# Optimization experiments

Hardware: AMD Instinct MI355X
Metric: run time of the kernel (lower is better)

The kernel has to match this reference:

```python
import jax, jax.numpy as jnp
import numpy as np

B, C, L = 32, 8, 2048
K, S = 512, 64  # num_shapelets, shapelets_size


def setup_inputs() -> dict:
    key = jax.random.key(0)
    k1, k2 = jax.random.split(key)
    x = jax.random.normal(k1, (B, C, L), dtype=jnp.float32)
    shapelets = jax.random.normal(k2, (C, K, S), dtype=jnp.float32)
    return {"x": x, "shapelets": shapelets}


def reference(x, shapelets):
    # x: [B, C, L]; shapelets: [C, K, S]
    s = shapelets.shape[-1]
    n_dims = x.shape[1]
    W = x.shape[2] - s + 1  # number of sliding windows
    # unfold(2, S, 1): gather overlapping windows -> [B, C, W, S]
    idx = jnp.arange(W)[:, None] + jnp.arange(s)[None, :]
    xw = x[:, :, idx]
    # L2-normalize windows along window length (clamp min like torch)
    xw = xw / jnp.maximum(jnp.linalg.norm(xw, axis=-1, keepdims=True), 1e-8)
    # L2-normalize shapelets along length
    sn = shapelets / jnp.maximum(jnp.linalg.norm(shapelets, axis=-1, keepdims=True), 1e-8)
    # matmul [B,C,W,S] @ [C,S,K] then sum over C, fused into one einsum -> [B, W, K]
    sim = jnp.einsum('bcws,cks->bwk', xw, sn) / n_dims
    sim = jax.nn.relu(sim)
    # max over window positions -> [B, K]; keep the singleton channel dim like torch ([B,1,K])
    out = jnp.max(sim, axis=1)
    return out[:, None, :]
```

## Files before the change

### kernel.cpp

```cpp
#include <hip/hip_runtime.h>


#define B_ 32
#define C_ 8
#define L_ 2048
#define K_ 512
#define S_ 64
#define W_ 1985
#define XS_ 2176

typedef _Float16 f16x8  __attribute__((ext_vector_type(8)));
typedef _Float16 f16x8u __attribute__((ext_vector_type(8), aligned(4)));
typedef float    f32x16 __attribute__((ext_vector_type(16)));

__global__ __launch_bounds__(256)
void prep_k(const float* __restrict__ x, const float* __restrict__ sh,
            _Float16* __restrict__ Bp, float* __restrict__ invn,
            _Float16* __restrict__ xh0, _Float16* __restrict__ xh1,
            float* __restrict__ out) {
    __shared__ float xr[L_];
    const int tid = threadIdx.x;
    const int blk = blockIdx.x;

    if (blk < 128) {
        const int sb   = blk * 4 + (tid >> 6);
        const int c    = sb >> 6;
        const int kq   = (sb >> 4) & 3;
        const int nt   = sb & 15;
        const int lane = tid & 63;
        const int half = lane >> 5;
        const int q    = nt * 32 + (lane & 31);

        const float4* sp = (const float4*)(sh + (size_t)(c * K_ + q) * S_);
        float ss = 0.f;
        #pragma unroll
        for (int i = 0; i < 8; ++i) {
            float4 v = sp[half * 8 + i];
            ss += v.x * v.x + v.y * v.y + v.z * v.z + v.w * v.w;
        }
        ss += __shfl_xor(ss, 32);
        float inv = 1.f / fmaxf(sqrtf(ss), 1e-8f);

        float4 u0 = sp[kq * 4 + half * 2];
        float4 u1 = sp[kq * 4 + half * 2 + 1];
        f16x8 o;
        o[0] = (_Float16)(u0.x * inv); o[1] = (_Float16)(u0.y * inv);
        o[2] = (_Float16)(u0.z * inv); o[3] = (_Float16)(u0.w * inv);
        o[4] = (_Float16)(u1.x * inv); o[5] = (_Float16)(u1.y * inv);
        o[6] = (_Float16)(u1.z * inv); o[7] = (_Float16)(u1.w * inv);
        ((f16x8*)Bp)[((c * 4 + kq) * 16 + nt) * 64 + lane] = o;
    } else {
        const int r = blk - 128;
        const float* xp = x + (size_t)r * L_;
        for (int i = tid; i < L_ / 4; i += 256)
            ((float4*)xr)[i] = ((const float4*)xp)[i];
        __syncthreads();

        float* ivp = invn + (size_t)r * L_;
        const int w0 = tid * 8;
        float ss = 0.f;
        if (w0 < W_) {
            #pragma unroll
            for (int j = 0; j < S_; ++j) { float v = xr[w0 + j]; ss += v * v; }
        }
        #pragma unroll
        for (int u = 0; u < 8; ++u) {
            int w = w0 + u;
            float o = 0.f;
            if (u > 0 && w < W_)
                ss += xr[w + 63] * xr[w + 63] - xr[w - 1] * xr[w - 1];
            if (w < W_) o = 0.125f / fmaxf(sqrtf(ss), 1e-8f);
            if (w < L_) ivp[w] = o;
        }

        _Float16* p0 = xh0 + (size_t)r * XS_;
        _Float16* p1 = xh1 + (size_t)r * XS_;
        for (int i = tid; i < XS_ / 8; i += 256) {
            f16x8 o0, o1;
            #pragma unroll
            for (int j = 0; j < 8; ++j) {
                int e = i * 8 + j;
                o0[j] = (_Float16)((e     < L_) ? xr[e]     : 0.f);
                o1[j] = (_Float16)((e + 1 < L_) ? xr[e + 1] : 0.f);
            }
            ((f16x8*)p0)[i] = o0;
            ((f16x8*)p1)[i] = o1;
        }
        if (r < 64) out[r * 256 + tid] = 0.f;
    }
}

__device__ __forceinline__ void glds16(const void* g, void* l) {
    __builtin_amdgcn_global_load_lds(
        (const __attribute__((address_space(1))) unsigned int*)g,
        (__attribute__((address_space(3))) unsigned int*)l, 16, 0, 0);
}

__device__ __forceinline__ void loadA(
    int c, const _Float16* __restrict__ xbase, const float* __restrict__ ivbase,
    int m0, int m1, f16x8 (&ar)[8], float (&iv)[2])
{
    iv[0] = ivbase[(size_t)c * L_ + m0];
    iv[1] = ivbase[(size_t)c * L_ + m1];
    const _Float16* xp = xbase + (size_t)c * XS_;
    #pragma unroll
    for (int mt = 0; mt < 2; ++mt)
        #pragma unroll
        for (int ks = 0; ks < 4; ++ks)
            ar[mt * 4 + ks] = *(const f16x8u*)(xp + mt * 32 + ks * 16);
}

__device__ __forceinline__ void compC(
    const f16x8* __restrict__ bsl, int lane, int nw,
    const f16x8 (&ar)[8], const float (&iv)[2], f32x16 (&acc)[2][2])
{
    f16x8 bf[8];
    #pragma unroll
    for (int ks = 0; ks < 4; ++ks)
        #pragma unroll
        for (int nt = 0; nt < 2; ++nt)
            bf[ks * 2 + nt] = bsl[(ks * 4 + nw * 2 + nt) * 64 + lane];

    const _Float16 h0 = (_Float16)iv[0], h1 = (_Float16)iv[1];
    f16x8 is0, is1;
    #pragma unroll
    for (int j = 0; j < 8; ++j) { is0[j] = h0; is1[j] = h1; }

    #pragma unroll
    for (int ks = 0; ks < 4; ++ks) {
        f16x8 a0 = ar[0 * 4 + ks] * is0;
        f16x8 a1 = ar[1 * 4 + ks] * is1;
        #pragma unroll
        for (int nt = 0; nt < 2; ++nt) {
            acc[0][nt] = __builtin_amdgcn_mfma_f32_32x32x16_f16(
                a0, bf[ks * 2 + nt], acc[0][nt], 0, 0, 0);
            acc[1][nt] = __builtin_amdgcn_mfma_f32_32x32x16_f16(
                a1, bf[ks * 2 + nt], acc[1][nt], 0, 0, 0);
        }
    }
}

__global__ __launch_bounds__(256, 2)
void mcs_k(const _Float16* __restrict__ xh0, const _Float16* __restrict__ xh1,
           const _Float16* __restrict__ Bp, const float* __restrict__ invn,
           float* __restrict__ out) {
    const int wt  = blockIdx.x;
    const int ng  = blockIdx.y;
    const int b   = blockIdx.z;
    const int tid = threadIdx.x;
    const int lane = tid & 63;
    const int wv   = tid >> 6;
    const int mg   = wv >> 1;
    const int nw   = wv & 1;

    const int l31 = lane & 31;
    const int lh  = lane >> 5;
    const int Wb  = wt * 128 + mg * 64;
    const int m0  = Wb + l31;
    const int m1  = Wb + 32 + l31;

    __shared__ f16x8 Bs[2][16][64];
    __shared__ float red[2][2][32];

    const _Float16* xb = (l31 & 1) ? (xh1 - 1) : xh0;
    const _Float16* xbase = xb + (size_t)b * C_ * XS_ + Wb + l31 + lh * 8;
    const float*   ivbase = invn + (size_t)b * C_ * L_;
    const f16x8*   sg = (const f16x8*)Bp + ((wv * 16 + ng * 4) * 64) + lane;

    f32x16 acc[2][2];
    #pragma unroll
    for (int mt = 0; mt < 2; ++mt)
        #pragma unroll
        for (int nt = 0; nt < 2; ++nt)
            #pragma unroll
            for (int r = 0; r < 16; ++r) acc[mt][nt][r] = 0.f;

    f16x8 aA[8], aB[8];
    float ivA[2], ivB[2];

    #define STAGE(c, buf)                                              \
        { _Pragma("unroll")                                            \
          for (int u = 0; u < 4; ++u)                                  \
              glds16(sg + ((c) * 64 + u) * 64, &Bs[buf][wv * 4 + u][0]); }

    STAGE(0, 0);
    loadA(0, xbase, ivbase, m0, m1, aA, ivA);
    __syncthreads();

    #pragma unroll 1
    for (int cp = 0; cp < 4; ++cp) {
        const int c0 = cp * 2;
        STAGE(c0 + 1, 1);
        loadA(c0 + 1, xbase, ivbase, m0, m1, aB, ivB);
        compC(&Bs[0][0][0], lane, nw, aA, ivA, acc);
        __syncthreads();
        if (cp < 3) {
            STAGE(c0 + 2, 0);
            loadA(c0 + 2, xbase, ivbase, m0, m1, aA, ivA);
        }
        compC(&Bs[1][0][0], lane, nw, aB, ivB, acc);
        __syncthreads();
    }
    #undef STAGE

    float m[2];
    #pragma unroll
    for (int nt = 0; nt < 2; ++nt) {
        float v = 0.f;
        #pragma unroll
        for (int mt = 0; mt < 2; ++mt)
            #pragma unroll
            for (int r = 0; r < 16; ++r) v = fmaxf(v, acc[mt][nt][r]);
        v = fmaxf(v, __shfl_xor(v, 32));
        m[nt] = v;
    }

    if (mg == 0 && lane < 32) {
        red[nw][0][l31] = m[0];
        red[nw][1][l31] = m[1];
    }
    __syncthreads();
    if (mg == 1 && lane < 32) {
        #pragma unroll
        for (int nt = 0; nt < 2; ++nt) {
            float v = fmaxf(m[nt], red[nw][nt][l31]);
            atomicMax((unsigned int*)(out + (size_t)b * K_ + ng * 128 + nw * 64 + nt * 32 + l31),
                      __float_as_uint(v));
        }
    }
}

extern "C" void kernel_launch(void* const* d_in, const int* in_sizes, int n_in,
                              void* d_out, int out_size, void* d_ws, size_t ws_size,
                              hipStream_t stream) {
    const float* x  = (const float*)d_in[0];
    const float* sh = (const float*)d_in[1];
    float* out = (float*)d_out;

    _Float16* Bp   = (_Float16*)d_ws;
    float*    invn = (float*)((char*)d_ws + (512 << 10));
    _Float16* xh0  = (_Float16*)((char*)d_ws + (512 << 10) + (2 << 20));
    _Float16* xh1  = xh0 + (size_t)B_ * C_ * XS_;

    prep_k<<<dim3(384), dim3(256), 0, stream>>>(x, sh, Bp, invn, xh0, xh1, out);
    mcs_k<<<dim3(16, 4, B_), dim3(256), 0, stream>>>(xh0, xh1, Bp, invn, out);
}
```

Before: 99.50 us.

## Preload all-channel shapelet tile to LDS once and drop per-channel barriers

Each block now handles 256 windows by 64 shapelets. Every wave owns 64 windows and all 64 shapelets of the block, so no cross-wave reduction is needed. The shapelet B fragments for all 8 channels (64 KB) are loaded into LDS once at the start, which removes the per-channel double-buffered staging and the two __syncthreads per channel pair. MFMA sections are wrapped in s_setprio to favour matrix issue. The costs are more LDS per block, which may limit occupancy, and twice as many atomicMax writes, one per wave instead of a shared reduction.

```diff
diff --git a/kernel.cpp b/kernel.cpp
--- a/kernel.cpp
+++ b/kernel.cpp
@@ -111,7 +111,7 @@
 }
 
 __device__ __forceinline__ void compC(
-    const f16x8* __restrict__ bsl, int lane, int nw,
+    int c, const f16x8* __restrict__ bsl, int lane,
     const f16x8 (&ar)[8], const float (&iv)[2], f32x16 (&acc)[2][2])
 {
     f16x8 bf[8];
@@ -119,13 +119,14 @@
     for (int ks = 0; ks < 4; ++ks)
         #pragma unroll
         for (int nt = 0; nt < 2; ++nt)
-            bf[ks * 2 + nt] = bsl[(ks * 4 + nw * 2 + nt) * 64 + lane];
+            bf[ks * 2 + nt] = bsl[(c * 8 + ks * 2 + nt) * 64 + lane];
 
     const _Float16 h0 = (_Float16)iv[0], h1 = (_Float16)iv[1];
     f16x8 is0, is1;
     #pragma unroll
     for (int j = 0; j < 8; ++j) { is0[j] = h0; is1[j] = h1; }
 
+    __builtin_amdgcn_s_setprio(1);
     #pragma unroll
     for (int ks = 0; ks < 4; ++ks) {
         f16x8 a0 = ar[0 * 4 + ks] * is0;
@@ -138,6 +139,7 @@
                 a1, bf[ks * 2 + nt], acc[1][nt], 0, 0, 0);
         }
     }
+    __builtin_amdgcn_s_setprio(0);
 }
 
 __global__ __launch_bounds__(256, 2)
@@ -150,22 +152,30 @@
     const int tid = threadIdx.x;
     const int lane = tid & 63;
     const int wv   = tid >> 6;
-    const int mg   = wv >> 1;
-    const int nw   = wv & 1;
 
     const int l31 = lane & 31;
     const int lh  = lane >> 5;
-    const int Wb  = wt * 128 + mg * 64;
+    const int Wb  = wt * 256 + wv * 64;
     const int m0  = Wb + l31;
     const int m1  = Wb + 32 + l31;
 
-    __shared__ f16x8 Bs[2][16][64];
-    __shared__ float red[2][2][32];
+    __shared__ f16x8 Bs[64][64];
+
+    {
+        const f16x8* bp = (const f16x8*)Bp;
+        #pragma unroll
+        for (int u = 0; u < 16; ++u) {
+            const int e   = wv * 16 + u;
+            const int c   = e >> 3;
+            const int sub = e & 7;
+            const int src = ((c * 4 + (sub >> 1)) * 16 + ng * 2 + (sub & 1)) * 64;
+            glds16(bp + src + lane, &Bs[e][0]);
+        }
+    }
 
     const _Float16* xb = (l31 & 1) ? (xh1 - 1) : xh0;
     const _Float16* xbase = xb + (size_t)b * C_ * XS_ + Wb + l31 + lh * 8;
     const float*   ivbase = invn + (size_t)b * C_ * L_;
-    const f16x8*   sg = (const f16x8*)Bp + ((wv * 16 + ng * 4) * 64) + lane;
 
     f32x16 acc[2][2];
     #pragma unroll
@@ -178,32 +188,19 @@
     f16x8 aA[8], aB[8];
     float ivA[2], ivB[2];
 
-    #define STAGE(c, buf)                                              \
-        { _Pragma("unroll")                                            \
-          for (int u = 0; u < 4; ++u)                                  \
-              glds16(sg + ((c) * 64 + u) * 64, &Bs[buf][wv * 4 + u][0]); }
-
-    STAGE(0, 0);
     loadA(0, xbase, ivbase, m0, m1, aA, ivA);
     __syncthreads();
 
     #pragma unroll 1
     for (int cp = 0; cp < 4; ++cp) {
         const int c0 = cp * 2;
-        STAGE(c0 + 1, 1);
         loadA(c0 + 1, xbase, ivbase, m0, m1, aB, ivB);
-        compC(&Bs[0][0][0], lane, nw, aA, ivA, acc);
-        __syncthreads();
-        if (cp < 3) {
-            STAGE(c0 + 2, 0);
+        compC(c0, &Bs[0][0], lane, aA, ivA, acc);
+        if (cp < 3)
             loadA(c0 + 2, xbase, ivbase, m0, m1, aA, ivA);
-        }
-        compC(&Bs[1][0][0], lane, nw, aB, ivB, acc);
-        __syncthreads();
-    }
-    #undef STAGE
-
-    float m[2];
+        compC(c0 + 1, &Bs[0][0], lane, aB, ivB, acc);
+    }
+
     #pragma unroll
     for (int nt = 0; nt < 2; ++nt) {
         float v = 0.f;
@@ -212,21 +209,9 @@
             #pragma unroll
             for (int r = 0; r < 16; ++r) v = fmaxf(v, acc[mt][nt][r]);
         v = fmaxf(v, __shfl_xor(v, 32));
-        m[nt] = v;
-    }
-
-    if (mg == 0 && lane < 32) {
-        red[nw][0][l31] = m[0];
-        red[nw][1][l31] = m[1];
-    }
-    __syncthreads();
-    if (mg == 1 && lane < 32) {
-        #pragma unroll
-        for (int nt = 0; nt < 2; ++nt) {
-            float v = fmaxf(m[nt], red[nw][nt][l31]);
-            atomicMax((unsigned int*)(out + (size_t)b * K_ + ng * 128 + nw * 64 + nt * 32 + l31),
+        if (lane < 32)
+            atomicMax((unsigned int*)(out + (size_t)b * K_ + ng * 64 + nt * 32 + l31),
                       __float_as_uint(v));
-        }
     }
 }
 
@@ -243,5 +228,5 @@
     _Float16* xh1  = xh0 + (size_t)B_ * C_ * XS_;
 
     prep_k<<<dim3(384), dim3(256), 0, stream>>>(x, sh, Bp, invn, xh0, xh1, out);
-    mcs_k<<<dim3(16, 4, B_), dim3(256), 0, stream>>>(xh0, xh1, Bp, invn, out);
-}
+    mcs_k<<<dim3(8, 8, B_), dim3(256), 0, stream>>>(xh0, xh1, Bp, invn, out);
+}
```

Result: no change. 98.81 us (-0.7%).
